# Optimization experiments

Hardware: AMD Instinct MI355X
Metric: run time of the kernel (lower is better)

## Reference

```python
import jax, jax.numpy as jnp
import numpy as np

N, E, D, MAX_L = 8192, 8192, 128, 16


def setup_inputs() -> dict:
    key = jax.random.key(0)
    k_x, k_inc, k_ord, k_w, k_b = jax.random.split(key, 5)
    x = jax.random.normal(k_x, (N, D), dtype=jnp.float32)
    # sparse-ish binary incidence matrix (n nodes x e hyperedges)
    incidence = (jax.random.uniform(k_inc, (N, E)) < 0.01).astype(jnp.float32)
    edge_orders = jax.random.randint(k_ord, (E,), 0, MAX_L + 1)
    # per-edge normalizer = number of incident nodes (avoid div-by-zero)
    prefix_normalizer = incidence.sum(axis=0) + 1.0
    # Positional2DWeight table: (2, max_l+1, dim_in, dim_out)
    W = jax.random.normal(k_w, (2, MAX_L + 1, D, D), dtype=jnp.float32) * (1.0 / np.sqrt(D))
    # PositionalWeight bias table: (max_l+1, dim_out)
    B = jax.random.normal(k_b, (MAX_L + 1, D), dtype=jnp.float32) * 0.02
    return {"x": x, "incidence": incidence, "edge_orders": edge_orders,
            "prefix_normalizer": prefix_normalizer, "W": W, "B": B}


def reference(x, incidence, edge_orders, prefix_normalizer, W, B):
    # order-indexed weight gather: (e, d, d) each
    w0 = W[0][edge_orders]
    w1 = W[1][edge_orders]
    # order-1 weights for the node-side update: (d, d)
    w0_1 = W[0, 1]
    w1_1 = W[1, 1]
    # global mean feature (order-0 term): (d,)
    x0 = x.mean(axis=0)
    # incidence aggregation: mean of incident node features per edge: (e, d)
    x1_e = (incidence.T @ x) / prefix_normalizer[:, None]
    # node output: broadcast order-0 term + per-node linear
    x_v = x0 @ w0_1 + x @ w1_1                      # (n, d)
    # edge output: per-edge matmul with order-gathered weights
    x_e = jnp.einsum('i,eij->ej', x0, w0) + jnp.einsum('ei,eij->ej', x1_e, w1)  # (e, d)
    # biases: order-gathered for edges, order-1 for nodes
    b = B[edge_orders]                               # (e, d)
    b_1 = B[1]                                       # (d,)
    return (x_v + b_1, x_e + b)
```

## Files before the change

kernel.cpp:

```cpp
#include <hip/hip_runtime.h>
#include <stdint.h>

#define NN 8192
#define NE 8192
#define DIM 128
#define NL 17
#define SPLITK 8
#define KCHUNK (NN / SPLITK)
#define NIT64 (KCHUNK / 64)

typedef float f32x4 __attribute__((ext_vector_type(4)));
typedef short short8 __attribute__((ext_vector_type(8)));

#define WS_XHI    0ull
#define WS_COLSUM (4ull << 20)
#define WS_C0E    ((4ull << 20) + (64ull << 10))
#define WS_WP     (5ull << 20)
#define WS_PART   (8ull << 20)

#define GPTR(p) ((const __attribute__((address_space(1))) uint32_t*)(p))
#define LPTR(p) ((__attribute__((address_space(3))) uint32_t*)(p))

__device__ __forceinline__ uint16_t f32_to_bf16(float v) {
  uint32_t u = __builtin_bit_cast(uint32_t, v);
  u += 0x7fffu + ((u >> 16) & 1u);
  return (uint16_t)(u >> 16);
}

__global__ __launch_bounds__(256) void k_prep(const float* __restrict__ x,
                                              uint16_t* __restrict__ xhi,
                                              float* __restrict__ colsum) {
  __shared__ float xs[64][129];
  const int t = threadIdx.x;
  const int b = blockIdx.x;
  const float4* xg = (const float4*)(x + (size_t)b * 64 * DIM);
  for (int r = 0; r < 8; ++r) {
    int f = t + r * 256;
    float4 v = xg[f];
    int n = f >> 5;
    int d0 = (f & 31) * 4;
    xs[n][d0] = v.x; xs[n][d0 + 1] = v.y; xs[n][d0 + 2] = v.z; xs[n][d0 + 3] = v.w;
  }
  __syncthreads();
  if (t < 128) {
    float s = 0.f;
    for (int n = 0; n < 64; ++n) s += xs[n][t];
    colsum[b * DIM + t] = s;
  }
  for (int r = 0; r < 4; ++r) {
    int q = t + r * 256;
    int c = q & 3;
    int d = (q >> 2) & 127;
    int kb = q >> 9;
    int kk0 = c * 8;
    uint32_t w[4];
    for (int j = 0; j < 4; ++j) {
      uint16_t h0 = f32_to_bf16(xs[kb * 32 + kk0 + 2 * j][d]);
      uint16_t h1 = f32_to_bf16(xs[kb * 32 + kk0 + 2 * j + 1][d]);
      w[j] = (uint32_t)h0 | ((uint32_t)h1 << 16);
    }
    int kblk = b * 2 + kb;
    uint16_t* dst = xhi + ((size_t)(kblk * 128 + d)) * 32 + kk0;
    *(uint4*)dst = make_uint4(w[0], w[1], w[2], w[3]);
  }
}

__global__ __launch_bounds__(128) void k_aux(const float* __restrict__ colsum,
                                             const float* __restrict__ W,
                                             const float* __restrict__ Bb,
                                             float* __restrict__ c0e,
                                             uint32_t* __restrict__ Wp) {
  __shared__ float x0[DIM];
  const int j = threadIdx.x;
  const int bid = blockIdx.x;
  if (bid < 17) {
    float s = 0.f;
    for (int b = 0; b < 128; ++b) s += colsum[b * DIM + j];
    x0[j] = s * (1.0f / NN);
    __syncthreads();
    const int l = bid;
    const float* W0l = W + (size_t)l * DIM * DIM;
    float acc = Bb[l * DIM + j];
#pragma unroll 8
    for (int i = 0; i < DIM; ++i) acc += x0[i] * W0l[(size_t)i * DIM + j];
    c0e[l * DIM + j] = acc;
  } else {
    const int l = bid - 17;
    const float* W1l = W + (size_t)(NL + l) * DIM * DIM;
    uint32_t* dst = Wp + (size_t)l * 64 * DIM;
#pragma unroll 8
    for (int i2 = 0; i2 < 64; ++i2) {
      uint16_t lo = f32_to_bf16(W1l[(size_t)(2 * i2) * DIM + j]);
      uint16_t hi = f32_to_bf16(W1l[(size_t)(2 * i2 + 1) * DIM + j]);
      dst[i2 * DIM + j] = (uint32_t)lo | ((uint32_t)hi << 16);
    }
  }
}

__global__ __launch_bounds__(256, 2) void k_gemm(const float* __restrict__ inc,
                                                 const uint16_t* __restrict__ xhi,
                                                 uint32_t* __restrict__ part16) {
  __shared__ uint16_t Bs[2][8192];
  const int t = threadIdx.x;
  const int mb = blockIdx.x & 63;
  const int s = blockIdx.x >> 6;
  const int e0 = mb * 128;
  const int w = t >> 6;
  const int lane = t & 63;
  const int lm = lane & 15;
  const int lk = lane >> 4;
  const int kbase = s * KCHUNK;
  const int kb0 = kbase >> 5;

  f32x4 acc[2][8];
#pragma unroll
  for (int a = 0; a < 2; ++a)
#pragma unroll
    for (int b = 0; b < 8; ++b) acc[a][b] = (f32x4){0.f, 0.f, 0.f, 0.f};

  const char* hbase = (const char*)xhi;

#define STAGE(buf, it) { \
    const char* hsrc = hbase + (size_t)(kb0 + 2 * (it)) * 8192; \
    char* dbase = (char*)&Bs[buf][0]; \
    _Pragma("unroll") \
    for (int j = 0; j < 4; ++j) { \
      int q = w + 4 * j; \
      __builtin_amdgcn_global_load_lds(GPTR(hsrc + q * 1024 + lane * 16), \
                                       LPTR(dbase + q * 1024), 16, 0, 0); \
    } }

#define LOADA(u, it) { \
    _Pragma("unroll") \
    for (int kh = 0; kh < 2; ++kh) { \
      const int k0_ = kbase + (it) * 64 + kh * 32; \
      _Pragma("unroll") \
      for (int fm = 0; fm < 2; ++fm) { \
        const float* ap = inc + (size_t)(k0_ + lk * 8) * NE + (e0 + w * 32 + fm * 16 + lm); \
        _Pragma("unroll") \
        for (int j = 0; j < 8; ++j) \
          u[fm][kh * 8 + j] = __builtin_bit_cast(uint32_t, ap[(size_t)j * NE]); \
      } \
    } }

#define COMPUTE(buf, u) { \
    _Pragma("unroll") \
    for (int kh = 0; kh < 2; ++kh) { \
      short8 afr[2]; \
      _Pragma("unroll") \
      for (int fm = 0; fm < 2; ++fm) { \
        union { uint32_t w4[4]; short8 s8; } pk; \
        _Pragma("unroll") \
        for (int j = 0; j < 4; ++j) \
          pk.w4[j] = (u[fm][kh * 8 + 2 * j + 1] & 0xffff0000u) | \
                     (u[fm][kh * 8 + 2 * j] >> 16); \
        afr[fm] = pk.s8; \
      } \
      _Pragma("unroll") \
      for (int fn = 0; fn < 8; ++fn) { \
        int n = fn * 16 + lm; \
        short8 bh = *(const short8*)&Bs[buf][kh * 4096 + n * 32 + lk * 8]; \
        acc[0][fn] = __builtin_amdgcn_mfma_f32_16x16x32_bf16(afr[0], bh, acc[0][fn], 0, 0, 0); \
        acc[1][fn] = __builtin_amdgcn_mfma_f32_16x16x32_bf16(afr[1], bh, acc[1][fn], 0, 0, 0); \
      } \
    } }

#define BAR() __builtin_amdgcn_s_barrier()
#define WAITK() { asm volatile("s_waitcnt vmcnt(36)" ::: "memory"); \
                  __builtin_amdgcn_sched_barrier(0); }
#define WAIT0() { asm volatile("s_waitcnt vmcnt(0)" ::: "memory"); \
                  __builtin_amdgcn_sched_barrier(0); }

  uint32_t ua[2][16], ub[2][16];
  STAGE(0, 0);
  LOADA(ua, 0);

  for (int it2 = 0; it2 < NIT64; it2 += 2) {
    if (it2 + 1 < NIT64) { STAGE(1, it2 + 1); LOADA(ub, it2 + 1); WAITK(); }
    else { WAIT0(); }
    BAR();
    COMPUTE(0, ua);
    BAR();
    if (it2 + 2 < NIT64) { STAGE(0, it2 + 2); LOADA(ua, it2 + 2); WAITK(); }
    else { WAIT0(); }
    BAR();
    COMPUTE(1, ub);
    BAR();
  }

  uint32_t* pbase = part16 + (size_t)s * NE * 64;
#pragma unroll
  for (int fm = 0; fm < 2; ++fm)
#pragma unroll
    for (int r = 0; r < 4; ++r) {
      int e = e0 + w * 32 + fm * 16 + lk * 4 + r;
#pragma unroll
      for (int j = 0; j < 4; ++j) {
        uint32_t pv = (uint32_t)f32_to_bf16(acc[fm][2 * j][r]) |
                      ((uint32_t)f32_to_bf16(acc[fm][2 * j + 1][r]) << 16);
        pbase[(size_t)e * 64 + j * 16 + lm] = pv;
      }
    }
#undef STAGE
#undef LOADA
#undef COMPUTE
#undef BAR
#undef WAITK
#undef WAIT0
}

__global__ __launch_bounds__(128) void k_edge2(const uint32_t* __restrict__ part16,
                                               const int* __restrict__ orders,
                                               const float* __restrict__ norm,
                                               const uint32_t* __restrict__ Wp,
                                               const float* __restrict__ c0e,
                                               float* __restrict__ out_e) {
  __shared__ float xl[DIM];
  const int t = threadIdx.x;
  const int e = blockIdx.x;
  if (t < 64) {
    const int d0 = 32 * (t >> 4) + (t & 15);
    float s0 = 0.f, s1 = 0.f;
#pragma unroll
    for (int k = 0; k < SPLITK; ++k) {
      uint32_t v = part16[((size_t)k * NE + e) * 64 + t];
      s0 += __builtin_bit_cast(float, v << 16);
      s1 += __builtin_bit_cast(float, v & 0xffff0000u);
    }
    const float rn = norm[e];
    xl[d0] = s0 / rn;
    xl[d0 + 16] = s1 / rn;
  }
  __syncthreads();
  const int l = orders[e];
  const uint32_t* Wl = Wp + (size_t)l * 64 * DIM;
  float o = c0e[l * DIM + t];
#pragma unroll 8
  for (int i2 = 0; i2 < 64; ++i2) {
    uint32_t wv = Wl[i2 * DIM + t];
    float wlo = __builtin_bit_cast(float, wv << 16);
    float whi = __builtin_bit_cast(float, wv & 0xffff0000u);
    o += xl[2 * i2] * wlo;
    o += xl[2 * i2 + 1] * whi;
  }
  out_e[(size_t)e * DIM + t] = o;
}

__global__ __launch_bounds__(256) void k_node(const float* __restrict__ x,
                                              const float* __restrict__ W,
                                              const float* __restrict__ c0e,
                                              float* __restrict__ out_v) {
  __shared__ float xr[32][DIM];
  const int t = threadIdx.x;
  const int row0 = blockIdx.x * 32;
  for (int i = t; i < 32 * DIM; i += 256)
    xr[i >> 7][i & 127] = x[(size_t)row0 * DIM + i];
  const int tx = t & 31;
  const int ty = t >> 5;
  const float4* W4 = (const float4*)(W + (size_t)(NL + 1) * DIM * DIM);
  const float4 cv = ((const float4*)(c0e + DIM))[tx];
  float4 o0 = cv, o1 = cv, o2 = cv, o3 = cv;
  __syncthreads();
#pragma unroll 4
  for (int k = 0; k < DIM; ++k) {
    float4 w = W4[k * 32 + tx];
    float a0 = xr[ty * 4 + 0][k];
    float a1 = xr[ty * 4 + 1][k];
    float a2 = xr[ty * 4 + 2][k];
    float a3 = xr[ty * 4 + 3][k];
    o0.x += a0 * w.x; o0.y += a0 * w.y; o0.z += a0 * w.z; o0.w += a0 * w.w;
    o1.x += a1 * w.x; o1.y += a1 * w.y; o1.z += a1 * w.z; o1.w += a1 * w.w;
    o2.x += a2 * w.x; o2.y += a2 * w.y; o2.z += a2 * w.z; o2.w += a2 * w.w;
    o3.x += a3 * w.x; o3.y += a3 * w.y; o3.z += a3 * w.z; o3.w += a3 * w.w;
  }
  float4* out4 = (float4*)(out_v + (size_t)(row0 + ty * 4) * DIM);
  out4[0 * 32 + tx] = o0;
  out4[1 * 32 + tx] = o1;
  out4[2 * 32 + tx] = o2;
  out4[3 * 32 + tx] = o3;
}

extern "C" void kernel_launch(void* const* d_in, const int* in_sizes, int n_in,
                              void* d_out, int out_size, void* d_ws, size_t ws_size,
                              hipStream_t stream) {
  const float* x      = (const float*)d_in[0];
  const float* inc    = (const float*)d_in[1];
  const int*   orders = (const int*)d_in[2];
  const float* norm   = (const float*)d_in[3];
  const float* W      = (const float*)d_in[4];
  const float* Bb     = (const float*)d_in[5];
  float* out_v = (float*)d_out;
  float* out_e = (float*)d_out + (size_t)NN * DIM;

  char* ws = (char*)d_ws;
  uint16_t* xhi   = (uint16_t*)(ws + WS_XHI);
  float* colsum   = (float*)(ws + WS_COLSUM);
  float* c0e      = (float*)(ws + WS_C0E);
  uint32_t* Wp    = (uint32_t*)(ws + WS_WP);
  uint32_t* part16 = (uint32_t*)(ws + WS_PART);

  k_prep<<<128, 256, 0, stream>>>(x, xhi, colsum);
  k_aux<<<34, 128, 0, stream>>>(colsum, W, Bb, c0e, Wp);
  k_gemm<<<512, 256, 0, stream>>>(inc, xhi, part16);
  k_edge2<<<NE, 128, 0, stream>>>(part16, orders, norm, Wp, c0e, out_e);
  k_node<<<NN / 32, 256, 0, stream>>>(x, W, c0e, out_v);
}
```

Baseline: 97.00 us.

## Fold aux work into GEMM launch and merge edge and node kernels

The small k_aux work (computing c0e and packing W1 to bf16) now runs as 34 extra blocks appended to the k_gemm grid. The separate k_edge2 and k_node kernels are merged into one launch, with node blocks resized from 32 rows/256 threads to 16 rows/128 threads. This cuts two kernel launches and lets the independent node work overlap with the edge tail. The aux blocks in the GEMM launch still depend on colsum from k_prep, which is fine because stream order is kept.

```diff
diff --git a/kernel.cpp b/kernel.cpp
--- a/kernel.cpp
+++ b/kernel.cpp
@@ -65,43 +65,52 @@
   }
 }
 
-__global__ __launch_bounds__(128) void k_aux(const float* __restrict__ colsum,
-                                             const float* __restrict__ W,
-                                             const float* __restrict__ Bb,
-                                             float* __restrict__ c0e,
-                                             uint32_t* __restrict__ Wp) {
-  __shared__ float x0[DIM];
-  const int j = threadIdx.x;
-  const int bid = blockIdx.x;
-  if (bid < 17) {
-    float s = 0.f;
-    for (int b = 0; b < 128; ++b) s += colsum[b * DIM + j];
-    x0[j] = s * (1.0f / NN);
-    __syncthreads();
-    const int l = bid;
-    const float* W0l = W + (size_t)l * DIM * DIM;
-    float acc = Bb[l * DIM + j];
-#pragma unroll 8
-    for (int i = 0; i < DIM; ++i) acc += x0[i] * W0l[(size_t)i * DIM + j];
-    c0e[l * DIM + j] = acc;
-  } else {
-    const int l = bid - 17;
-    const float* W1l = W + (size_t)(NL + l) * DIM * DIM;
-    uint32_t* dst = Wp + (size_t)l * 64 * DIM;
-#pragma unroll 8
-    for (int i2 = 0; i2 < 64; ++i2) {
-      uint16_t lo = f32_to_bf16(W1l[(size_t)(2 * i2) * DIM + j]);
-      uint16_t hi = f32_to_bf16(W1l[(size_t)(2 * i2 + 1) * DIM + j]);
-      dst[i2 * DIM + j] = (uint32_t)lo | ((uint32_t)hi << 16);
-    }
-  }
-}
-
 __global__ __launch_bounds__(256, 2) void k_gemm(const float* __restrict__ inc,
                                                  const uint16_t* __restrict__ xhi,
-                                                 uint32_t* __restrict__ part16) {
+                                                 uint32_t* __restrict__ part16,
+                                                 const float* __restrict__ colsum,
+                                                 const float* __restrict__ W,
+                                                 const float* __restrict__ Bb,
+                                                 float* __restrict__ c0e,
+                                                 uint32_t* __restrict__ Wp) {
   __shared__ uint16_t Bs[2][8192];
   const int t = threadIdx.x;
+
+  if (blockIdx.x >= 512) {
+    const int bid2 = blockIdx.x - 512;
+    if (bid2 < 17) {
+      __shared__ float x0[DIM];
+      if (t < 128) {
+        float s = 0.f;
+        for (int b = 0; b < 128; ++b) s += colsum[b * DIM + t];
+        x0[t] = s * (1.0f / NN);
+      }
+      __syncthreads();
+      if (t < 128) {
+        const int l = bid2;
+        const float* W0l = W + (size_t)l * DIM * DIM;
+        float acc = Bb[l * DIM + t];
+#pragma unroll 8
+        for (int i = 0; i < DIM; ++i) acc += x0[i] * W0l[(size_t)i * DIM + t];
+        c0e[l * DIM + t] = acc;
+      }
+    } else {
+      const int l = bid2 - 17;
+      const int j = t & 127;
+      const int half = t >> 7;
+      const float* W1l = W + (size_t)(NL + l) * DIM * DIM;
+      uint32_t* dst = Wp + (size_t)l * 64 * DIM;
+#pragma unroll 8
+      for (int q = 0; q < 32; ++q) {
+        int i2 = half * 32 + q;
+        uint16_t lo = f32_to_bf16(W1l[(size_t)(2 * i2) * DIM + j]);
+        uint16_t hi = f32_to_bf16(W1l[(size_t)(2 * i2 + 1) * DIM + j]);
+        dst[i2 * DIM + j] = (uint32_t)lo | ((uint32_t)hi << 16);
+      }
+    }
+    return;
+  }
+
   const int mb = blockIdx.x & 63;
   const int s = blockIdx.x >> 6;
   const int e0 = mb * 128;
@@ -209,75 +218,78 @@
 #undef WAIT0
 }
 
-__global__ __launch_bounds__(128) void k_edge2(const uint32_t* __restrict__ part16,
-                                               const int* __restrict__ orders,
-                                               const float* __restrict__ norm,
-                                               const uint32_t* __restrict__ Wp,
-                                               const float* __restrict__ c0e,
-                                               float* __restrict__ out_e) {
-  __shared__ float xl[DIM];
+__global__ __launch_bounds__(128) void k_edgenode(const uint32_t* __restrict__ part16,
+                                                  const int* __restrict__ orders,
+                                                  const float* __restrict__ norm,
+                                                  const uint32_t* __restrict__ Wp,
+                                                  const float* __restrict__ c0e,
+                                                  const float* __restrict__ x,
+                                                  const float* __restrict__ W,
+                                                  float* __restrict__ out_e,
+                                                  float* __restrict__ out_v) {
+  __shared__ float sh[16 * DIM];
   const int t = threadIdx.x;
-  const int e = blockIdx.x;
-  if (t < 64) {
-    const int d0 = 32 * (t >> 4) + (t & 15);
-    float s0 = 0.f, s1 = 0.f;
-#pragma unroll
-    for (int k = 0; k < SPLITK; ++k) {
-      uint32_t v = part16[((size_t)k * NE + e) * 64 + t];
-      s0 += __builtin_bit_cast(float, v << 16);
-      s1 += __builtin_bit_cast(float, v & 0xffff0000u);
-    }
-    const float rn = norm[e];
-    xl[d0] = s0 / rn;
-    xl[d0 + 16] = s1 / rn;
-  }
-  __syncthreads();
-  const int l = orders[e];
-  const uint32_t* Wl = Wp + (size_t)l * 64 * DIM;
-  float o = c0e[l * DIM + t];
+  if (blockIdx.x < NE) {
+    const int e = blockIdx.x;
+    if (t < 64) {
+      const int d0 = 32 * (t >> 4) + (t & 15);
+      float s0 = 0.f, s1 = 0.f;
+#pragma unroll
+      for (int k = 0; k < SPLITK; ++k) {
+        uint32_t v = part16[((size_t)k * NE + e) * 64 + t];
+        s0 += __builtin_bit_cast(float, v << 16);
+        s1 += __builtin_bit_cast(float, v & 0xffff0000u);
+      }
+      const float rn = norm[e];
+      sh[d0] = s0 / rn;
+      sh[d0 + 16] = s1 / rn;
+    }
+    __syncthreads();
+    const int l = orders[e];
+    const uint32_t* Wl = Wp + (size_t)l * 64 * DIM;
+    float o = c0e[l * DIM + t];
 #pragma unroll 8
-  for (int i2 = 0; i2 < 64; ++i2) {
-    uint32_t wv = Wl[i2 * DIM + t];
-    float wlo = __builtin_bit_cast(float, wv << 16);
-    float whi = __builtin_bit_cast(float, wv & 0xffff0000u);
-    o += xl[2 * i2] * wlo;
-    o += xl[2 * i2 + 1] * whi;
-  }
-  out_e[(size_t)e * DIM + t] = o;
-}
-
-__global__ __launch_bounds__(256) void k_node(const float* __restrict__ x,
-                                              const float* __restrict__ W,
-                                              const float* __restrict__ c0e,
-                                              float* __restrict__ out_v) {
-  __shared__ float xr[32][DIM];
-  const int t = threadIdx.x;
-  const int row0 = blockIdx.x * 32;
-  for (int i = t; i < 32 * DIM; i += 256)
-    xr[i >> 7][i & 127] = x[(size_t)row0 * DIM + i];
-  const int tx = t & 31;
-  const int ty = t >> 5;
-  const float4* W4 = (const float4*)(W + (size_t)(NL + 1) * DIM * DIM);
-  const float4 cv = ((const float4*)(c0e + DIM))[tx];
-  float4 o0 = cv, o1 = cv, o2 = cv, o3 = cv;
-  __syncthreads();
+    for (int i2 = 0; i2 < 64; ++i2) {
+      uint32_t wv = Wl[i2 * DIM + t];
+      float wlo = __builtin_bit_cast(float, wv << 16);
+      float whi = __builtin_bit_cast(float, wv & 0xffff0000u);
+      o += sh[2 * i2] * wlo;
+      o += sh[2 * i2 + 1] * whi;
+    }
+    out_e[(size_t)e * DIM + t] = o;
+  } else {
+    const int nb = blockIdx.x - NE;
+    const int row0 = nb * 16;
+    {
+      const float4* xg = (const float4*)(x + (size_t)row0 * DIM);
+      float4* sh4 = (float4*)sh;
+#pragma unroll
+      for (int r = 0; r < 4; ++r) sh4[t + r * 128] = xg[t + r * 128];
+    }
+    const int tx = t & 31;
+    const int ty = t >> 5;
+    const float4* W4 = (const float4*)(W + (size_t)(NL + 1) * DIM * DIM);
+    const float4 cv = ((const float4*)(c0e + DIM))[tx];
+    float4 o0 = cv, o1 = cv, o2 = cv, o3 = cv;
+    __syncthreads();
 #pragma unroll 4
-  for (int k = 0; k < DIM; ++k) {
-    float4 w = W4[k * 32 + tx];
-    float a0 = xr[ty * 4 + 0][k];
-    float a1 = xr[ty * 4 + 1][k];
-    float a2 = xr[ty * 4 + 2][k];
-    float a3 = xr[ty * 4 + 3][k];
-    o0.x += a0 * w.x; o0.y += a0 * w.y; o0.z += a0 * w.z; o0.w += a0 * w.w;
-    o1.x += a1 * w.x; o1.y += a1 * w.y; o1.z += a1 * w.z; o1.w += a1 * w.w;
-    o2.x += a2 * w.x; o2.y += a2 * w.y; o2.z += a2 * w.z; o2.w += a2 * w.w;
-    o3.x += a3 * w.x; o3.y += a3 * w.y; o3.z += a3 * w.z; o3.w += a3 * w.w;
-  }
-  float4* out4 = (float4*)(out_v + (size_t)(row0 + ty * 4) * DIM);
-  out4[0 * 32 + tx] = o0;
-  out4[1 * 32 + tx] = o1;
-  out4[2 * 32 + tx] = o2;
-  out4[3 * 32 + tx] = o3;
+    for (int k = 0; k < DIM; ++k) {
+      float4 w = W4[k * 32 + tx];
+      float a0 = sh[(ty * 4 + 0) * DIM + k];
+      float a1 = sh[(ty * 4 + 1) * DIM + k];
+      float a2 = sh[(ty * 4 + 2) * DIM + k];
+      float a3 = sh[(ty * 4 + 3) * DIM + k];
+      o0.x += a0 * w.x; o0.y += a0 * w.y; o0.z += a0 * w.z; o0.w += a0 * w.w;
+      o1.x += a1 * w.x; o1.y += a1 * w.y; o1.z += a1 * w.z; o1.w += a1 * w.w;
+      o2.x += a2 * w.x; o2.y += a2 * w.y; o2.z += a2 * w.z; o2.w += a2 * w.w;
+      o3.x += a3 * w.x; o3.y += a3 * w.y; o3.z += a3 * w.z; o3.w += a3 * w.w;
+    }
+    float4* out4 = (float4*)(out_v + (size_t)(row0 + ty * 4) * DIM);
+    out4[0 * 32 + tx] = o0;
+    out4[1 * 32 + tx] = o1;
+    out4[2 * 32 + tx] = o2;
+    out4[3 * 32 + tx] = o3;
+  }
 }
 
 extern "C" void kernel_launch(void* const* d_in, const int* in_sizes, int n_in,
@@ -293,15 +305,14 @@
   float* out_e = (float*)d_out + (size_t)NN * DIM;
 
   char* ws = (char*)d_ws;
-  uint16_t* xhi   = (uint16_t*)(ws + WS_XHI);
-  float* colsum   = (float*)(ws + WS_COLSUM);
-  float* c0e      = (float*)(ws + WS_C0E);
-  uint32_t* Wp    = (uint32_t*)(ws + WS_WP);
+  uint16_t* xhi    = (uint16_t*)(ws + WS_XHI);
+  float* colsum    = (float*)(ws + WS_COLSUM);
+  float* c0e       = (float*)(ws + WS_C0E);
+  uint32_t* Wp     = (uint32_t*)(ws + WS_WP);
   uint32_t* part16 = (uint32_t*)(ws + WS_PART);
 
   k_prep<<<128, 256, 0, stream>>>(x, xhi, colsum);
-  k_aux<<<34, 128, 0, stream>>>(colsum, W, Bb, c0e, Wp);
-  k_gemm<<<512, 256, 0, stream>>>(inc, xhi, part16);
-  k_edge2<<<NE, 128, 0, stream>>>(part16, orders, norm, Wp, c0e, out_e);
-  k_node<<<NN / 32, 256, 0, stream>>>(x, W, c0e, out_v);
-}
+  k_gemm<<<546, 256, 0, stream>>>(inc, xhi, part16, colsum, W, Bb, c0e, Wp);
+  k_edgenode<<<NE + 512, 128, 0, stream>>>(part16, orders, norm, Wp, c0e, x, W,
+                                           out_e, out_v);
+}
```

Measured after the change: 90.98 us. -6.2%, faster.
